# Optimization experiments

Hardware: AMD Instinct MI355X
Metric: run time of the kernel (lower is better)

Reference implementation:

```python
import jax, jax.numpy as jnp
import numpy as np

B, N, H, W = 4, 4096, 480, 640
RADIUS = 2.0        # hard-coded self.radius in DiskLoss
SCORES_TH = 0.1     # PeakyLoss scores_th
KP_PENALTY = -0.001 # configs['kp_penalty']


def setup_inputs() -> dict:
    key = jax.random.key(0)
    ks = jax.random.split(key, 6)
    lp0 = jax.random.uniform(ks[0], (B, 1, H, W), dtype=jnp.float32)
    lp1 = jax.random.uniform(ks[1], (B, 1, H, W), dtype=jnp.float32)
    # keypoints are normalized grid_sample coords in [-1, 1], (x, y) order
    kp0 = jax.random.uniform(ks[2], (B, N, 2), dtype=jnp.float32) * 2.0 - 1.0
    kp1 = jax.random.uniform(ks[3], (B, N, 2), dtype=jnp.float32) * 2.0 - 1.0
    d0 = jax.random.uniform(ks[4], (B, N), dtype=jnp.float32)
    d1 = jax.random.uniform(ks[5], (B, N), dtype=jnp.float32)
    return dict(local_point0=lp0, local_point1=lp1, keypoints0=kp0,
                keypoints1=kp1, score_dispersity0=d0, score_dispersity1=d1)


def grid_sample_bilinear(img, pts):
    """torch.grid_sample(mode='bilinear', align_corners=True) for one image.
    img: [H, W]; pts: [N, 2] in [-1, 1], pts[:,0]=x (width), pts[:,1]=y (height)."""
    Hh, Ww = img.shape
    x = (pts[:, 0] + 1.0) * 0.5 * (Ww - 1)
    y = (pts[:, 1] + 1.0) * 0.5 * (Hh - 1)
    x0 = jnp.floor(x); y0 = jnp.floor(y)
    wx = x - x0; wy = y - y0
    def g(yy, xx):
        yi = jnp.clip(yy, 0, Hh - 1).astype(jnp.int32)
        xi = jnp.clip(xx, 0, Ww - 1).astype(jnp.int32)
        return img[yi, xi]
    return (g(y0, x0) * (1 - wx) * (1 - wy)
            + g(y0, x0 + 1) * wx * (1 - wy)
            + g(y0 + 1, x0) * (1 - wx) * wy
            + g(y0 + 1, x0 + 1) * wx * wy)


def nms_valid(kpts_wh, scores):
    """Faithful sequential NMS from compute_correspondence for one image.
    kpts_wh: [N, 2] pixel coords; scores: [N]. Returns bool [N] valid mask."""
    n = scores.shape[0]
    sq = jnp.sum(kpts_wh * kpts_wh, axis=-1)
    d2 = sq[:, None] + sq[None, :] - 2.0 * (kpts_wh @ kpts_wh.T)  # [N, N]
    local_mask = d2 < RADIUS * RADIUS
    valid_cnt0 = local_mask.sum(-1).astype(jnp.int32)
    need = valid_cnt0 > 1  # indices_need_nms (computed once, as in torch)
    idx = jnp.arange(n)
    neg_inf = jnp.asarray(-jnp.inf, scores.dtype)
    def body(i, vc):
        row = local_mask[i]
        cond = need[i] & (vc[i] > 0)
        j = jnp.argmax(jnp.where(row, scores, neg_inf))  # best-scoring neighbor
        suppressed = jnp.where(row & (idx != j), 0, vc)
        return jnp.where(cond, suppressed, vc)
    vc = jax.lax.fori_loop(0, n, body, valid_cnt0)
    return vc > 0


def stream_loss(local_point, kpts, disp):
    # local_point [B,1,H,W], kpts [B,N,2] in [-1,1], disp [B,N]
    wh = jnp.array([local_point.shape[3] - 1, local_point.shape[2] - 1],
                   dtype=local_point.dtype)
    scores = jax.vmap(lambda m, k: grid_sample_bilinear(m[0], k))(local_point, kpts)  # [B,N]
    kpts_wh = (kpts / 2.0 + 0.5) * wh  # pixel coords
    valid = jax.vmap(nms_valid)(jax.lax.stop_gradient(kpts_wh),
                                jax.lax.stop_gradient(scores))  # [B,N] bool
    # PeakyLoss over NMS-surviving keypoints with score > threshold
    peaky_mask = (valid & (scores > SCORES_TH)).astype(disp.dtype)
    cnt = jnp.maximum(peaky_mask.sum(), 1.0)
    loss_peaky = jnp.sum(disp * peaky_mask) / cnt
    # keypoint score term (kp_penalty-weighted mean of surviving scores)
    vmask = valid.astype(scores.dtype)
    vcnt = jnp.maximum(vmask.sum(), 1.0)
    score_mean = jnp.sum(scores * vmask) / vcnt
    return loss_peaky + KP_PENALTY * score_mean


def reference(local_point0, local_point1, keypoints0, keypoints1,
              score_dispersity0, score_dispersity1):
    return (stream_loss(local_point0, keypoints0, score_dispersity0)
            + stream_loss(local_point1, keypoints1, score_dispersity1))
```

## Files before the change

### kernel.cpp

```cpp
#include <hip/hip_runtime.h>
#include <math.h>

#define NN 4096
#define HH 480
#define WW 640
#define RAD2 4.0f
#define TH_SCORE 0.1f
#define KPPEN -0.001f
#define CXN 160
#define CYN 120
#define NCELL (CXN * CYN)
#define SLOTS 8
#define CAP 48

#define OFF_SCORES  0
#define OFF_PTS     131072
#define OFF_CNT     655360
#define OFF_PARTNER 688128
#define OFF_CELLS   753664
#define OFF_CCNT    3211264
#define OFF_ACC     3825664

__device__ __forceinline__ int cell_of(float x, float y, int img) {
    int cx = (int)(x * 0.25f); cx = cx < 0 ? 0 : (cx > CXN - 1 ? CXN - 1 : cx);
    int cy = (int)(y * 0.25f); cy = cy < 0 ? 0 : (cy > CYN - 1 ? CYN - 1 : cy);
    return img * NCELL + cy * CXN + cx;
}

__global__ __launch_bounds__(256) void k_sample(
    const float* __restrict__ lp0, const float* __restrict__ lp1,
    const float* __restrict__ kp0, const float* __restrict__ kp1,
    float* __restrict__ scores, float4* __restrict__ pts,
    unsigned short* __restrict__ cells, unsigned int* __restrict__ ccnt)
{
#pragma clang fp contract(off)
    int gid = blockIdx.x * 256 + threadIdx.x;
    int s = gid >> 14;
    int r = gid & 16383;
    int b = r >> 12;
    const float* kp  = (s ? kp1 : kp0) + (size_t)r * 2;
    const float* img = (s ? lp1 : lp0) + (size_t)b * (HH * WW);
    float px = kp[0], py = kp[1];
    float x = (px + 1.0f) * 0.5f * (float)(WW - 1);
    float y = (py + 1.0f) * 0.5f * (float)(HH - 1);
    float x0 = floorf(x), y0 = floorf(y);
    float wx = x - x0, wy = y - y0;
    int ix0 = (int)fminf(fmaxf(x0, 0.0f), (float)(WW - 1));
    int iy0 = (int)fminf(fmaxf(y0, 0.0f), (float)(HH - 1));
    int ix1 = (int)fminf(fmaxf(x0 + 1.0f, 0.0f), (float)(WW - 1));
    int iy1 = (int)fminf(fmaxf(y0 + 1.0f, 0.0f), (float)(HH - 1));
    float g00 = img[iy0 * WW + ix0];
    float g01 = img[iy0 * WW + ix1];
    float g10 = img[iy1 * WW + ix0];
    float g11 = img[iy1 * WW + ix1];
    float sc = g00 * (1.0f - wx) * (1.0f - wy)
             + g01 * wx * (1.0f - wy)
             + g10 * (1.0f - wx) * wy
             + g11 * wx * wy;
    float xw = (px / 2.0f + 0.5f) * (float)(WW - 1);
    float yw = (py / 2.0f + 0.5f) * (float)(HH - 1);
    float sq = xw * xw + yw * yw;
    scores[gid] = sc;
    pts[gid] = make_float4(xw, yw, sq, 0.0f);
    int imgid = gid >> 12;
    int li = gid & (NN - 1);
    int cell = cell_of(xw, yw, imgid);
    unsigned int pos = atomicAdd(&ccnt[cell], 1u);
    if (pos < SLOTS) cells[(size_t)cell * SLOTS + pos] = (unsigned short)li;
}

__global__ __launch_bounds__(256) void k_cnt(
    const float4* __restrict__ pts, const unsigned short* __restrict__ cells,
    const unsigned int* __restrict__ ccnt,
    unsigned char* __restrict__ cnt, unsigned short* __restrict__ partner)
{
#pragma clang fp contract(off)
    int gid = blockIdx.x * 256 + threadIdx.x;
    int imgid = gid >> 12;
    int li = gid & (NN - 1);
    const float4* p = pts + ((size_t)imgid << 12);
    float4 a = p[li];
    int cx = (int)(a.x * 0.25f); cx = cx < 0 ? 0 : (cx > CXN - 1 ? CXN - 1 : cx);
    int cy = (int)(a.y * 0.25f); cy = cy < 0 ? 0 : (cy > CYN - 1 ? CYN - 1 : cy);
    int c = 0, sum = 0; bool ov = false;
    for (int dy = -1; dy <= 1; ++dy) {
        int yy = cy + dy; if (yy < 0 || yy >= CYN) continue;
        for (int dx = -1; dx <= 1; ++dx) {
            int xx = cx + dx; if (xx < 0 || xx >= CXN) continue;
            int cell = imgid * NCELL + yy * CXN + xx;
            int n = (int)ccnt[cell];
            if (n > SLOTS) { ov = true; n = SLOTS; }
            for (int k = 0; k < n; ++k) {
                int q = cells[(size_t)cell * SLOTS + k];
                float4 qq = p[q];
                float dot = a.x * qq.x + a.y * qq.y;
                float t = a.z + qq.z;
                float d2 = fmaf(-2.0f, dot, t);
                if (d2 < RAD2) { ++c; sum += q; }
            }
        }
    }
    if (ov) {
        c = 0; sum = 0;
        for (int j = 0; j < NN; ++j) {
            float4 qq = p[j];
            float dot = a.x * qq.x + a.y * qq.y;
            float t = a.z + qq.z;
            float d2 = fmaf(-2.0f, dot, t);
            if (d2 < RAD2) { ++c; sum += j; }
        }
    }
    cnt[gid] = (unsigned char)(c > 255 ? 255 : c);
    partner[gid] = (unsigned short)((sum - li) & 0xFFFF);
}

__global__ __launch_bounds__(256) void k_nms(
    const float* __restrict__ scoresG, const float4* __restrict__ pts,
    const unsigned char* __restrict__ cntG, const unsigned short* __restrict__ partnerG,
    const unsigned short* __restrict__ cells, const unsigned int* __restrict__ ccnt,
    const float* __restrict__ dd0, const float* __restrict__ dd1,
    float* __restrict__ acc)
{
#pragma clang fp contract(off)
    __shared__ float          s_sc[NN];
    __shared__ unsigned char  s_cnt[NN];
    __shared__ unsigned short s_partner[NN];
    __shared__ unsigned short s_mem[256][CAP + 2];
    __shared__ unsigned short s_row[256][10];
    __shared__ float s_red[4];

    int imgid = blockIdx.x >> 4;
    int seg = blockIdx.x & 15;
    int base = imgid << 12;
    int tid = threadIdx.x;
    const float4* p = pts + (size_t)base;

    for (int t = tid; t < NN; t += 256) {
        s_sc[t] = scoresG[base + t];
        s_cnt[t] = cntG[base + t];
        s_partner[t] = partnerG[base + t];
    }
    __syncthreads();

    int li = (seg << 8) + tid;
    int c = s_cnt[li];
    bool alive = true;

    if (c >= 2) {
        int pr = s_partner[li];
        if (c == 2 && s_cnt[pr] == 2) {
            int lo = li < pr ? li : pr, hi = li < pr ? pr : li;
            int w = (s_sc[lo] >= s_sc[hi]) ? lo : hi;
            alive = (w == li);
        } else {
            unsigned short* mem = s_mem[tid];
            unsigned short* rb = s_row[tid];
            int cntm = 1, proc = 0;
            mem[0] = (unsigned short)li;
            auto insert = [&](int q) {
                for (int k = 0; k < cntm; ++k) if (mem[k] == (unsigned short)q) return;
                if (cntm < CAP) mem[cntm++] = (unsigned short)q;
            };
            auto gather = [&](int m, float4 pm) -> int {
                int gx = (int)(pm.x * 0.25f); gx = gx < 0 ? 0 : (gx > CXN - 1 ? CXN - 1 : gx);
                int gy = (int)(pm.y * 0.25f); gy = gy < 0 ? 0 : (gy > CYN - 1 ? CYN - 1 : gy);
                int rc = 0; bool ov = false;
                for (int dy = -1; dy <= 1; ++dy) {
                    int yy = gy + dy; if (yy < 0 || yy >= CYN) continue;
                    for (int dx = -1; dx <= 1; ++dx) {
                        int xx = gx + dx; if (xx < 0 || xx >= CXN) continue;
                        int cell = imgid * NCELL + yy * CXN + xx;
                        int n = (int)ccnt[cell];
                        if (n > SLOTS) { ov = true; n = SLOTS; }
                        for (int k = 0; k < n; ++k) {
                            int q = cells[(size_t)cell * SLOTS + k];
                            float4 qq = p[q];
                            float dot = pm.x * qq.x + pm.y * qq.y;
                            float t = pm.z + qq.z;
                            float d2 = fmaf(-2.0f, dot, t);
                            if (d2 < RAD2) { if (rc < 8) rb[rc] = (unsigned short)q; ++rc; }
                        }
                    }
                }
                return (ov || rc > 8) ? -1 : rc;
            };
            while (proc < cntm) {
                int m = mem[proc++];
                int cm = s_cnt[m];
                if (cm == 2) {
                    insert(s_partner[m]);
                } else if (cm <= 8) {
                    float4 pm = p[m];
                    int rc = gather(m, pm);
                    if (rc >= 0) {
                        for (int k = 0; k < rc; ++k) insert(rb[k]);
                    } else {
                        for (int j = 0; j < NN; ++j) {
                            float4 qq = p[j];
                            float dot = pm.x * qq.x + pm.y * qq.y;
                            float t = pm.z + qq.z;
                            float d2 = fmaf(-2.0f, dot, t);
                            if (d2 < RAD2) insert(j);
                        }
                    }
                } else {
                    float4 pm = p[m];
                    for (int j = 0; j < NN; ++j) {
                        float4 qq = p[j];
                        float dot = pm.x * qq.x + pm.y * qq.y;
                        float t = pm.z + qq.z;
                        float d2 = fmaf(-2.0f, dot, t);
                        if (d2 < RAD2) insert(j);
                    }
                }
            }
            for (int k = 1; k < cntm; ++k) {
                unsigned short v = mem[k]; int j2 = k;
                while (j2 > 0 && mem[j2 - 1] > v) { mem[j2] = mem[j2 - 1]; --j2; }
                mem[j2] = v;
            }
            unsigned long long am = (cntm >= 64) ? ~0ull : ((1ull << cntm) - 1ull);
            auto clearbit = [&](int q) {
                for (int k = 0; k < cntm; ++k)
                    if (mem[k] == (unsigned short)q) { am &= ~(1ull << k); return; }
            };
            for (int k = 0; k < cntm; ++k) {
                if (!((am >> k) & 1ull)) continue;
                int m = mem[k];
                int cm = s_cnt[m];
                if (cm == 2) {
                    int pr2 = s_partner[m];
                    int lo = m < pr2 ? m : pr2, hi = m < pr2 ? pr2 : m;
                    int w = (s_sc[lo] >= s_sc[hi]) ? lo : hi;
                    clearbit(w == lo ? hi : lo);
                } else if (cm <= 8) {
                    float4 pm = p[m];
                    int rc = gather(m, pm);
                    if (rc >= 0) {
                        float bs = -1.0f; int bi = NN;
                        for (int k2 = 0; k2 < rc; ++k2) {
                            int q = rb[k2]; float sc2 = s_sc[q];
                            if (sc2 > bs || (sc2 == bs && q < bi)) { bs = sc2; bi = q; }
                        }
                        for (int k2 = 0; k2 < rc; ++k2) {
                            int q = rb[k2];
                            if (q != bi) clearbit(q);
                        }
                    } else {
                        float bs = -1.0f; int bi = NN;
                        for (int j = 0; j < NN; ++j) {
                            float4 qq = p[j];
                            float dot = pm.x * qq.x + pm.y * qq.y;
                            float t = pm.z + qq.z;
                            float d2 = fmaf(-2.0f, dot, t);
                            if (d2 < RAD2) { float sc2 = s_sc[j];
                                if (sc2 > bs || (sc2 == bs && j < bi)) { bs = sc2; bi = j; } }
                        }
                        for (int j = 0; j < NN; ++j) {
                            float4 qq = p[j];
                            float dot = pm.x * qq.x + pm.y * qq.y;
                            float t = pm.z + qq.z;
                            float d2 = fmaf(-2.0f, dot, t);
                            if (d2 < RAD2 && j != bi) clearbit(j);
                        }
                    }
                } else {
                    float4 pm = p[m];
                    float bs = -1.0f; int bi = NN;
                    for (int j = 0; j < NN; ++j) {
                        float4 qq = p[j];
                        float dot = pm.x * qq.x + pm.y * qq.y;
                        float t = pm.z + qq.z;
                        float d2 = fmaf(-2.0f, dot, t);
                        if (d2 < RAD2) { float sc2 = s_sc[j];
                            if (sc2 > bs || (sc2 == bs && j < bi)) { bs = sc2; bi = j; } }
                    }
                    for (int j = 0; j < NN; ++j) {
                        float4 qq = p[j];
                        float dot = pm.x * qq.x + pm.y * qq.y;
                        float t = pm.z + qq.z;
                        float d2 = fmaf(-2.0f, dot, t);
                        if (d2 < RAD2 && j != bi) clearbit(j);
                    }
                }
            }
            for (int k = 0; k < cntm; ++k)
                if (mem[k] == (unsigned short)li) { alive = ((am >> k) & 1ull) != 0; break; }
        }
    }

    int stream = imgid >> 2, b = imgid & 3;
    const float* disp = (stream ? dd1 : dd0) + (size_t)b * NN;
    float sum_dp = 0.f, cnt_p = 0.f, sum_sv = 0.f, cnt_v = 0.f;
    if (alive) {
        float sc = s_sc[li];
        cnt_v = 1.0f; sum_sv = sc;
        if (sc > TH_SCORE) { cnt_p = 1.0f; sum_dp = disp[li]; }
    }
    __syncthreads();
#pragma unroll
    for (int q = 0; q < 4; ++q) {
        float v = (q == 0) ? sum_dp : (q == 1) ? cnt_p : (q == 2) ? sum_sv : cnt_v;
        for (int o = 32; o > 0; o >>= 1) v += __shfl_down(v, o, 64);
        if ((tid & 63) == 0) s_red[tid >> 6] = v;
        __syncthreads();
        if (tid == 0) {
            float r = s_red[0] + s_red[1] + s_red[2] + s_red[3];
            atomicAdd(&acc[stream * 4 + q], r);
        }
        __syncthreads();
    }
}

__global__ void k_final(const float* __restrict__ acc, float* __restrict__ out)
{
    float r = 0.0f;
    for (int s = 0; s < 2; ++s) {
        float sdp = acc[s * 4 + 0], cp = acc[s * 4 + 1];
        float ssv = acc[s * 4 + 2], cv = acc[s * 4 + 3];
        r += sdp / fmaxf(cp, 1.0f) + KPPEN * (ssv / fmaxf(cv, 1.0f));
    }
    out[0] = r;
}

extern "C" void kernel_launch(void* const* d_in, const int* in_sizes, int n_in,
                              void* d_out, int out_size, void* d_ws, size_t ws_size,
                              hipStream_t stream)
{
    const float* lp0 = (const float*)d_in[0];
    const float* lp1 = (const float*)d_in[1];
    const float* kp0 = (const float*)d_in[2];
    const float* kp1 = (const float*)d_in[3];
    const float* dd0 = (const float*)d_in[4];
    const float* dd1 = (const float*)d_in[5];

    char* ws = (char*)d_ws;
    float*          scores  = (float*)(ws + OFF_SCORES);
    float4*         pts     = (float4*)(ws + OFF_PTS);
    unsigned char*  cnt     = (unsigned char*)(ws + OFF_CNT);
    unsigned short* partner = (unsigned short*)(ws + OFF_PARTNER);
    unsigned short* cells   = (unsigned short*)(ws + OFF_CELLS);
    unsigned int*   ccnt    = (unsigned int*)(ws + OFF_CCNT);
    float*          acc     = (float*)(ws + OFF_ACC);

    hipMemsetAsync(ws + OFF_CCNT, 0, 614432, stream);
    k_sample<<<128, 256, 0, stream>>>(lp0, lp1, kp0, kp1, scores, pts, cells, ccnt);
    k_cnt<<<128, 256, 0, stream>>>(pts, cells, ccnt, cnt, partner);
    k_nms<<<128, 256, 0, stream>>>(scores, pts, cnt, partner, cells, ccnt, dd0, dd1, acc);
    k_final<<<1, 1, 0, stream>>>(acc, (float*)d_out);
}
```

Baseline: 135.4 us.

## Cache neighbour rows in k_cnt, reuse in NMS, fuse final reduction

k_cnt now packs up to eight neighbour indices per keypoint into a 16-byte row and writes it out. k_nms reads this row directly instead of re-gathering the 3x3 grid cells, which it did twice per member. The cell scan loads each cell's slots with one vector load and unrolls the neighbourhood loop. The separate k_final launch is removed: the last k_nms block, found through a done counter and threadfence, computes the output. This saves one launch but adds an atomic completion protocol and extra workspace.

```diff
diff --git a/kernel.cpp b/kernel.cpp
--- a/kernel.cpp
+++ b/kernel.cpp
@@ -17,15 +17,11 @@
 #define OFF_PTS     131072
 #define OFF_CNT     655360
 #define OFF_PARTNER 688128
-#define OFF_CELLS   753664
-#define OFF_CCNT    3211264
-#define OFF_ACC     3825664
-
-__device__ __forceinline__ int cell_of(float x, float y, int img) {
-    int cx = (int)(x * 0.25f); cx = cx < 0 ? 0 : (cx > CXN - 1 ? CXN - 1 : cx);
-    int cy = (int)(y * 0.25f); cy = cy < 0 ? 0 : (cy > CYN - 1 ? CYN - 1 : cy);
-    return img * NCELL + cy * CXN + cx;
-}
+#define OFF_ROWS    753664
+#define OFF_CELLS   1277952
+#define OFF_CCNT    3735552
+#define OFF_ACC     4349952
+#define OFF_DONE    4349984
 
 __global__ __launch_bounds__(256) void k_sample(
     const float* __restrict__ lp0, const float* __restrict__ lp1,
@@ -64,7 +60,9 @@
     pts[gid] = make_float4(xw, yw, sq, 0.0f);
     int imgid = gid >> 12;
     int li = gid & (NN - 1);
-    int cell = cell_of(xw, yw, imgid);
+    int cx = (int)(xw * 0.25f); cx = cx < 0 ? 0 : (cx > CXN - 1 ? CXN - 1 : cx);
+    int cy = (int)(yw * 0.25f); cy = cy < 0 ? 0 : (cy > CYN - 1 ? CYN - 1 : cy);
+    int cell = imgid * NCELL + cy * CXN + cx;
     unsigned int pos = atomicAdd(&ccnt[cell], 1u);
     if (pos < SLOTS) cells[(size_t)cell * SLOTS + pos] = (unsigned short)li;
 }
@@ -72,7 +70,8 @@
 __global__ __launch_bounds__(256) void k_cnt(
     const float4* __restrict__ pts, const unsigned short* __restrict__ cells,
     const unsigned int* __restrict__ ccnt,
-    unsigned char* __restrict__ cnt, unsigned short* __restrict__ partner)
+    unsigned char* __restrict__ cnt, unsigned short* __restrict__ partner,
+    uint4* __restrict__ rows4)
 {
 #pragma clang fp contract(off)
     int gid = blockIdx.x * 256 + threadIdx.x;
@@ -82,51 +81,82 @@
     float4 a = p[li];
     int cx = (int)(a.x * 0.25f); cx = cx < 0 ? 0 : (cx > CXN - 1 ? CXN - 1 : cx);
     int cy = (int)(a.y * 0.25f); cy = cy < 0 ? 0 : (cy > CYN - 1 ? CYN - 1 : cy);
+
     int c = 0, sum = 0; bool ov = false;
+    unsigned long long rlo = 0ull, rhi = 0ull;
+    auto place = [&](int pos, unsigned q) {
+        unsigned long long v = (unsigned long long)q;
+        switch (pos) {
+            case 0: rlo |= v;       break;
+            case 1: rlo |= v << 16; break;
+            case 2: rlo |= v << 32; break;
+            case 3: rlo |= v << 48; break;
+            case 4: rhi |= v;       break;
+            case 5: rhi |= v << 16; break;
+            case 6: rhi |= v << 32; break;
+            case 7: rhi |= v << 48; break;
+        }
+    };
+    auto test = [&](unsigned q) {
+        float4 qq = p[q];
+        float dot = a.x * qq.x + a.y * qq.y;
+        float t = a.z + qq.z;
+        float d2 = fmaf(-2.0f, dot, t);
+        if (d2 < RAD2) {
+            if (c < 8) place(c, q);
+            ++c; sum += (int)q;
+        }
+    };
+
+#pragma unroll
     for (int dy = -1; dy <= 1; ++dy) {
-        int yy = cy + dy; if (yy < 0 || yy >= CYN) continue;
+#pragma unroll
         for (int dx = -1; dx <= 1; ++dx) {
-            int xx = cx + dx; if (xx < 0 || xx >= CXN) continue;
-            int cell = imgid * NCELL + yy * CXN + xx;
-            int n = (int)ccnt[cell];
+            int yy = cy + dy, xx = cx + dx;
+            bool valid = (yy >= 0) & (yy < CYN) & (xx >= 0) & (xx < CXN);
+            int cell = imgid * NCELL + (valid ? yy * CXN + xx : 0);
+            unsigned n = valid ? ccnt[cell] : 0u;
             if (n > SLOTS) { ov = true; n = SLOTS; }
-            for (int k = 0; k < n; ++k) {
-                int q = cells[(size_t)cell * SLOTS + k];
-                float4 qq = p[q];
-                float dot = a.x * qq.x + a.y * qq.y;
-                float t = a.z + qq.z;
-                float d2 = fmaf(-2.0f, dot, t);
-                if (d2 < RAD2) { ++c; sum += q; }
-            }
+            uint4 cl = valid ? *(const uint4*)&cells[(size_t)cell * SLOTS]
+                             : make_uint4(0, 0, 0, 0);
+            unsigned q0 = cl.x & 0xffffu, q1 = cl.x >> 16;
+            unsigned q2 = cl.y & 0xffffu, q3 = cl.y >> 16;
+            unsigned q4 = cl.z & 0xffffu, q5 = cl.z >> 16;
+            unsigned q6 = cl.w & 0xffffu, q7 = cl.w >> 16;
+            if (n > 0) test(q0);
+            if (n > 1) test(q1);
+            if (n > 2) test(q2);
+            if (n > 3) test(q3);
+            if (n > 4) test(q4);
+            if (n > 5) test(q5);
+            if (n > 6) test(q6);
+            if (n > 7) test(q7);
         }
     }
     if (ov) {
-        c = 0; sum = 0;
-        for (int j = 0; j < NN; ++j) {
-            float4 qq = p[j];
-            float dot = a.x * qq.x + a.y * qq.y;
-            float t = a.z + qq.z;
-            float d2 = fmaf(-2.0f, dot, t);
-            if (d2 < RAD2) { ++c; sum += j; }
-        }
+        c = 0; sum = 0; rlo = 0ull; rhi = 0ull;
+        for (int j = 0; j < NN; ++j) test((unsigned)j);
     }
     cnt[gid] = (unsigned char)(c > 255 ? 255 : c);
     partner[gid] = (unsigned short)((sum - li) & 0xFFFF);
+    if (c >= 3 && c <= 8)
+        rows4[gid] = make_uint4((unsigned)rlo, (unsigned)(rlo >> 32),
+                                (unsigned)rhi, (unsigned)(rhi >> 32));
 }
 
 __global__ __launch_bounds__(256) void k_nms(
     const float* __restrict__ scoresG, const float4* __restrict__ pts,
     const unsigned char* __restrict__ cntG, const unsigned short* __restrict__ partnerG,
-    const unsigned short* __restrict__ cells, const unsigned int* __restrict__ ccnt,
+    const uint4* __restrict__ rows4,
     const float* __restrict__ dd0, const float* __restrict__ dd1,
-    float* __restrict__ acc)
+    float* __restrict__ acc, unsigned int* __restrict__ done,
+    float* __restrict__ out)
 {
 #pragma clang fp contract(off)
     __shared__ float          s_sc[NN];
     __shared__ unsigned char  s_cnt[NN];
     __shared__ unsigned short s_partner[NN];
     __shared__ unsigned short s_mem[256][CAP + 2];
-    __shared__ unsigned short s_row[256][10];
     __shared__ float s_red[4];
 
     int imgid = blockIdx.x >> 4;
@@ -154,35 +184,21 @@
             alive = (w == li);
         } else {
             unsigned short* mem = s_mem[tid];
-            unsigned short* rb = s_row[tid];
             int cntm = 1, proc = 0;
             mem[0] = (unsigned short)li;
-            auto insert = [&](int q) {
+            auto insert = [&](unsigned q) {
                 for (int k = 0; k < cntm; ++k) if (mem[k] == (unsigned short)q) return;
                 if (cntm < CAP) mem[cntm++] = (unsigned short)q;
             };
-            auto gather = [&](int m, float4 pm) -> int {
-                int gx = (int)(pm.x * 0.25f); gx = gx < 0 ? 0 : (gx > CXN - 1 ? CXN - 1 : gx);
-                int gy = (int)(pm.y * 0.25f); gy = gy < 0 ? 0 : (gy > CYN - 1 ? CYN - 1 : gy);
-                int rc = 0; bool ov = false;
-                for (int dy = -1; dy <= 1; ++dy) {
-                    int yy = gy + dy; if (yy < 0 || yy >= CYN) continue;
-                    for (int dx = -1; dx <= 1; ++dx) {
-                        int xx = gx + dx; if (xx < 0 || xx >= CXN) continue;
-                        int cell = imgid * NCELL + yy * CXN + xx;
-                        int n = (int)ccnt[cell];
-                        if (n > SLOTS) { ov = true; n = SLOTS; }
-                        for (int k = 0; k < n; ++k) {
-                            int q = cells[(size_t)cell * SLOTS + k];
-                            float4 qq = p[q];
-                            float dot = pm.x * qq.x + pm.y * qq.y;
-                            float t = pm.z + qq.z;
-                            float d2 = fmaf(-2.0f, dot, t);
-                            if (d2 < RAD2) { if (rc < 8) rb[rc] = (unsigned short)q; ++rc; }
-                        }
-                    }
+            auto full_insert = [&](int m) {
+                float4 pm = p[m];
+                for (int j = 0; j < NN; ++j) {
+                    float4 qq = p[j];
+                    float dot = pm.x * qq.x + pm.y * qq.y;
+                    float t = pm.z + qq.z;
+                    float d2 = fmaf(-2.0f, dot, t);
+                    if (d2 < RAD2) insert((unsigned)j);
                 }
-                return (ov || rc > 8) ? -1 : rc;
             };
             while (proc < cntm) {
                 int m = mem[proc++];
@@ -190,28 +206,21 @@
                 if (cm == 2) {
                     insert(s_partner[m]);
                 } else if (cm <= 8) {
-                    float4 pm = p[m];
-                    int rc = gather(m, pm);
-                    if (rc >= 0) {
-                        for (int k = 0; k < rc; ++k) insert(rb[k]);
-                    } else {
-                        for (int j = 0; j < NN; ++j) {
-                            float4 qq = p[j];
-                            float dot = pm.x * qq.x + pm.y * qq.y;
-                            float t = pm.z + qq.z;
-                            float d2 = fmaf(-2.0f, dot, t);
-                            if (d2 < RAD2) insert(j);
-                        }
-                    }
+                    uint4 w = rows4[base + m];
+                    unsigned q0 = w.x & 0xffffu, q1 = w.x >> 16;
+                    unsigned q2 = w.y & 0xffffu, q3 = w.y >> 16;
+                    unsigned q4 = w.z & 0xffffu, q5 = w.z >> 16;
+                    unsigned q6 = w.w & 0xffffu, q7 = w.w >> 16;
+                    if (cm > 0) insert(q0);
+                    if (cm > 1) insert(q1);
+                    if (cm > 2) insert(q2);
+                    if (cm > 3) insert(q3);
+                    if (cm > 4) insert(q4);
+                    if (cm > 5) insert(q5);
+                    if (cm > 6) insert(q6);
+                    if (cm > 7) insert(q7);
                 } else {
-                    float4 pm = p[m];
-                    for (int j = 0; j < NN; ++j) {
-                        float4 qq = p[j];
-                        float dot = pm.x * qq.x + pm.y * qq.y;
-                        float t = pm.z + qq.z;
-                        float d2 = fmaf(-2.0f, dot, t);
-                        if (d2 < RAD2) insert(j);
-                    }
+                    full_insert(m);
                 }
             }
             for (int k = 1; k < cntm; ++k) {
@@ -220,7 +229,7 @@
                 mem[j2] = v;
             }
             unsigned long long am = (cntm >= 64) ? ~0ull : ((1ull << cntm) - 1ull);
-            auto clearbit = [&](int q) {
+            auto clearbit = [&](unsigned q) {
                 for (int k = 0; k < cntm; ++k)
                     if (mem[k] == (unsigned short)q) { am &= ~(1ull << k); return; }
             };
@@ -232,38 +241,27 @@
                     int pr2 = s_partner[m];
                     int lo = m < pr2 ? m : pr2, hi = m < pr2 ? pr2 : m;
                     int w = (s_sc[lo] >= s_sc[hi]) ? lo : hi;
-                    clearbit(w == lo ? hi : lo);
+                    clearbit((unsigned)(w == lo ? hi : lo));
                 } else if (cm <= 8) {
-                    float4 pm = p[m];
-                    int rc = gather(m, pm);
-                    if (rc >= 0) {
-                        float bs = -1.0f; int bi = NN;
-                        for (int k2 = 0; k2 < rc; ++k2) {
-                            int q = rb[k2]; float sc2 = s_sc[q];
-                            if (sc2 > bs || (sc2 == bs && q < bi)) { bs = sc2; bi = q; }
+                    uint4 w = rows4[base + m];
+                    unsigned q0 = w.x & 0xffffu, q1 = w.x >> 16;
+                    unsigned q2 = w.y & 0xffffu, q3 = w.y >> 16;
+                    unsigned q4 = w.z & 0xffffu, q5 = w.z >> 16;
+                    unsigned q6 = w.w & 0xffffu, q7 = w.w >> 16;
+                    float bs = -1.0f; int bi = NN;
+                    auto cand = [&](int k2, unsigned q) {
+                        if (k2 < cm) {
+                            float s2 = s_sc[q];
+                            if (s2 > bs || (s2 == bs && (int)q < bi)) { bs = s2; bi = (int)q; }
                         }
-                        for (int k2 = 0; k2 < rc; ++k2) {
-                            int q = rb[k2];
-                            if (q != bi) clearbit(q);
-                        }
-                    } else {
-                        float bs = -1.0f; int bi = NN;
-                        for (int j = 0; j < NN; ++j) {
-                            float4 qq = p[j];
-                            float dot = pm.x * qq.x + pm.y * qq.y;
-                            float t = pm.z + qq.z;
-                            float d2 = fmaf(-2.0f, dot, t);
-                            if (d2 < RAD2) { float sc2 = s_sc[j];
-                                if (sc2 > bs || (sc2 == bs && j < bi)) { bs = sc2; bi = j; } }
-                        }
-                        for (int j = 0; j < NN; ++j) {
-                            float4 qq = p[j];
-                            float dot = pm.x * qq.x + pm.y * qq.y;
-                            float t = pm.z + qq.z;
-                            float d2 = fmaf(-2.0f, dot, t);
-                            if (d2 < RAD2 && j != bi) clearbit(j);
-                        }
-                    }
+                    };
+                    cand(0, q0); cand(1, q1); cand(2, q2); cand(3, q3);
+                    cand(4, q4); cand(5, q5); cand(6, q6); cand(7, q7);
+                    auto clr = [&](int k2, unsigned q) {
+                        if (k2 < cm && (int)q != bi) clearbit(q);
+                    };
+                    clr(0, q0); clr(1, q1); clr(2, q2); clr(3, q3);
+                    clr(4, q4); clr(5, q5); clr(6, q6); clr(7, q7);
                 } else {
                     float4 pm = p[m];
                     float bs = -1.0f; int bi = NN;
@@ -272,15 +270,17 @@
                         float dot = pm.x * qq.x + pm.y * qq.y;
                         float t = pm.z + qq.z;
                         float d2 = fmaf(-2.0f, dot, t);
-                        if (d2 < RAD2) { float sc2 = s_sc[j];
-                            if (sc2 > bs || (sc2 == bs && j < bi)) { bs = sc2; bi = j; } }
+                        if (d2 < RAD2) {
+                            float s2 = s_sc[j];
+                            if (s2 > bs || (s2 == bs && j < bi)) { bs = s2; bi = j; }
+                        }
                     }
                     for (int j = 0; j < NN; ++j) {
                         float4 qq = p[j];
                         float dot = pm.x * qq.x + pm.y * qq.y;
                         float t = pm.z + qq.z;
                         float d2 = fmaf(-2.0f, dot, t);
-                        if (d2 < RAD2 && j != bi) clearbit(j);
+                        if (d2 < RAD2 && j != bi) clearbit((unsigned)j);
                     }
                 }
             }
@@ -310,17 +310,22 @@
         }
         __syncthreads();
     }
-}
-
-__global__ void k_final(const float* __restrict__ acc, float* __restrict__ out)
-{
-    float r = 0.0f;
-    for (int s = 0; s < 2; ++s) {
-        float sdp = acc[s * 4 + 0], cp = acc[s * 4 + 1];
-        float ssv = acc[s * 4 + 2], cv = acc[s * 4 + 3];
-        r += sdp / fmaxf(cp, 1.0f) + KPPEN * (ssv / fmaxf(cv, 1.0f));
-    }
-    out[0] = r;
+
+    if (tid == 0) {
+        __threadfence();
+        unsigned prev = atomicAdd(done, 1u);
+        if (prev == 127u) {
+            float r = 0.0f;
+            for (int s = 0; s < 2; ++s) {
+                float sdp = atomicAdd(&acc[s * 4 + 0], 0.0f);
+                float cp  = atomicAdd(&acc[s * 4 + 1], 0.0f);
+                float ssv = atomicAdd(&acc[s * 4 + 2], 0.0f);
+                float cv  = atomicAdd(&acc[s * 4 + 3], 0.0f);
+                r += sdp / fmaxf(cp, 1.0f) + KPPEN * (ssv / fmaxf(cv, 1.0f));
+            }
+            out[0] = r;
+        }
+    }
 }
 
 extern "C" void kernel_launch(void* const* d_in, const int* in_sizes, int n_in,
@@ -339,13 +344,15 @@
     float4*         pts     = (float4*)(ws + OFF_PTS);
     unsigned char*  cnt     = (unsigned char*)(ws + OFF_CNT);
     unsigned short* partner = (unsigned short*)(ws + OFF_PARTNER);
+    uint4*          rows4   = (uint4*)(ws + OFF_ROWS);
     unsigned short* cells   = (unsigned short*)(ws + OFF_CELLS);
     unsigned int*   ccnt    = (unsigned int*)(ws + OFF_CCNT);
     float*          acc     = (float*)(ws + OFF_ACC);
-
-    hipMemsetAsync(ws + OFF_CCNT, 0, 614432, stream);
+    unsigned int*   done    = (unsigned int*)(ws + OFF_DONE);
+
+    hipMemsetAsync(ws + OFF_CCNT, 0, 614436, stream);
     k_sample<<<128, 256, 0, stream>>>(lp0, lp1, kp0, kp1, scores, pts, cells, ccnt);
-    k_cnt<<<128, 256, 0, stream>>>(pts, cells, ccnt, cnt, partner);
-    k_nms<<<128, 256, 0, stream>>>(scores, pts, cnt, partner, cells, ccnt, dd0, dd1, acc);
-    k_final<<<1, 1, 0, stream>>>(acc, (float*)d_out);
+    k_cnt<<<128, 256, 0, stream>>>(pts, cells, ccnt, cnt, partner, rows4);
+    k_nms<<<128, 256, 0, stream>>>(scores, pts, cnt, partner, rows4,
+                                   dd0, dd1, acc, done, (float*)d_out);
 }
```

Measured after the change: 116.3 us. -14.1%, faster.
